# Performance work log

Measured on AMD Instinct MI355X. Metric: run time of the kernel, lower is better.

Reference implementation:

```python
import jax, jax.numpy as jnp
import numpy as np

N, D, K = 100000, 512, 32
H1, H2 = 512, 256
LN2PI_2 = float(np.log(2.0 * np.pi) / 2.0)


def _glorot(key, shape):
    fan_in, fan_out = shape[0], shape[1]
    limit = np.sqrt(6.0 / (fan_in + fan_out))
    return jax.random.uniform(key, shape, jnp.float32, -limit, limit)


def setup_inputs() -> dict:
    key = jax.random.key(0)
    k0, k1, k2, k3 = jax.random.split(key, 4)
    return {
        "x": jax.random.normal(k0, (N, D), jnp.float32),
        "W1": _glorot(k1, (D, H1)),
        "b1": jnp.zeros((H1,), jnp.float32),
        "W2": _glorot(k2, (H1, H2)),
        "b2": jnp.zeros((H2,), jnp.float32),
        "W3": _glorot(k3, (H2, K)),
        "b3": jnp.zeros((K,), jnp.float32),
    }


def reference(x, W1, b1, W2, b2, W3, b3):
    # instance attention MLP: softplus hiddens, softmax output -> [N, K]
    h = jax.nn.softplus(x @ W1 + b1)
    h = jax.nn.softplus(h @ W2 + b2)
    att = jax.nn.softmax(h @ W3 + b3, axis=-1)

    att_sum = jnp.sum(att, axis=0)  # [K]
    # weighted mean: sum_n x[n,d] * att[n,k] / sum_n att[n,k]  -> [K, D]
    means = (att.T @ x) / att_sum[:, None]
    # weighted variance: E_w[x^2] - mean^2 (algebraic expansion of
    # sum_n (x - mean)^2 * att / sum att, avoids [N,K,D] intermediate)
    ex2 = (att.T @ (x * x)) / att_sum[:, None]  # [K, D]
    vars_ = ex2 - means * means

    # GMM diagonal log-likelihood, expanded to GEMM form:
    inv_v = 1.0 / vars_  # [K, D]
    maha = (x * x) @ inv_v.T - 2.0 * (x @ (means * inv_v).T) \
           + jnp.sum(means * means * inv_v, axis=-1)[None, :]  # [N, K]
    gmm_log = -0.5 * maha - 0.5 * jnp.sum(jnp.log(vars_), axis=-1)[None, :] - D * LN2PI_2
    return gmm_log, vars_
```

## Files before the change

### kernel.cpp

```cpp
#include <hip/hip_runtime.h>
#include <hip/hip_bf16.h>
#include <math.h>

#define NROWS 100000
#define DDIM  512
#define KCL   32
#define H1DIM 512
#define H2DIM 256
#define LN2PI_2 0.9189385332046727f
#define NCHUNK 196
#define NPAD  100352
#define NBLK  784

typedef __attribute__((ext_vector_type(8))) short short8;
typedef __attribute__((ext_vector_type(4))) short shortx4;
typedef __attribute__((ext_vector_type(4))) float floatx4;

__device__ __forceinline__ float softplus_f(float v) {
    return fmaxf(v, 0.f) + __logf(1.f + __expf(-fabsf(v)));
}

__device__ __forceinline__ unsigned short f2bf_rne(float f) {
    unsigned int u = __float_as_uint(f);
    return (unsigned short)((u + 0x7fffu + ((u >> 16) & 1u)) >> 16);
}

__device__ __forceinline__ float bf2f(short v) {
    return __uint_as_float(((unsigned int)(unsigned short)v) << 16);
}

__global__ __launch_bounds__(256) void cvt_x_bf16(
    const float* __restrict__ x, short* __restrict__ xb)
{
    size_t i = ((size_t)blockIdx.x * 256 + threadIdx.x) * 8;
    float4 f0 = *(const float4*)&x[i];
    float4 f1 = *(const float4*)&x[i + 4];
    short8 o;
    o[0] = (short)f2bf_rne(f0.x); o[1] = (short)f2bf_rne(f0.y);
    o[2] = (short)f2bf_rne(f0.z); o[3] = (short)f2bf_rne(f0.w);
    o[4] = (short)f2bf_rne(f1.x); o[5] = (short)f2bf_rne(f1.y);
    o[6] = (short)f2bf_rne(f1.z); o[7] = (short)f2bf_rne(f1.w);
    *(short8*)&xb[i] = o;
}

__global__ __launch_bounds__(256) void cvt_weightT(
    const float* __restrict__ W, int Kd, int Nc, short* __restrict__ BT)
{
    int idx = blockIdx.x * 256 + threadIdx.x;
    if (idx >= Kd * Nc) return;
    int n = idx % Nc, k = idx / Nc;
    BT[(size_t)n * Kd + k] = (short)f2bf_rne(W[idx]);
}

#define LDP 40
__global__ __launch_bounds__(256) void gemm_bf16_softplus(
    const short* __restrict__ A, const short* __restrict__ BT,
    const float* __restrict__ bias, void* __restrict__ Cptr,
    int M, int Nc, int Kd, int out_bf16)
{
    __shared__ short As[2][128 * LDP];
    __shared__ short Bs[2][128 * LDP];

    const int tid = threadIdx.x;
    const int lid = tid & 63;
    const int w = tid >> 6;
    const int lm = lid & 15;
    const int lq = lid >> 4;
    const int wrow = (w & 1) * 64;
    const int wcol = (w >> 1) * 64;

    const int row0 = blockIdx.y * 128;
    const int col0 = blockIdx.x * 128;

    const int sr = tid >> 2;
    const int sc = (tid & 3) << 3;

    int gr0 = row0 + sr;       if (gr0 >= M) gr0 = M - 1;
    int gr1 = row0 + 64 + sr;  if (gr1 >= M) gr1 = M - 1;
    const short* Ar0 = A + (size_t)gr0 * Kd + sc;
    const short* Ar1 = A + (size_t)gr1 * Kd + sc;
    const short* Br0 = BT + (size_t)(col0 + sr) * Kd + sc;
    const short* Br1 = BT + (size_t)(col0 + 64 + sr) * Kd + sc;

    floatx4 acc[4][4];
    #pragma unroll
    for (int i = 0; i < 4; i++)
        #pragma unroll
        for (int j = 0; j < 4; j++)
            acc[i][j] = (floatx4){0.f, 0.f, 0.f, 0.f};

    short8 pa0, pa1, pb0, pb1;
    pa0 = *(const short8*)Ar0;
    pa1 = *(const short8*)Ar1;
    pb0 = *(const short8*)Br0;
    pb1 = *(const short8*)Br1;

    const int nk = Kd >> 5;
    for (int kt = 0; kt < nk; kt++) {
        const int buf = kt & 1;
        *(short8*)&As[buf][sr * LDP + sc]        = pa0;
        *(short8*)&As[buf][(64 + sr) * LDP + sc] = pa1;
        *(short8*)&Bs[buf][sr * LDP + sc]        = pb0;
        *(short8*)&Bs[buf][(64 + sr) * LDP + sc] = pb1;
        if (kt + 1 < nk) {
            int ko = (kt + 1) << 5;
            pa0 = *(const short8*)(Ar0 + ko);
            pa1 = *(const short8*)(Ar1 + ko);
            pb0 = *(const short8*)(Br0 + ko);
            pb1 = *(const short8*)(Br1 + ko);
        }
        __syncthreads();

        short8 a[4], b[4];
        #pragma unroll
        for (int i = 0; i < 4; i++)
            a[i] = *(const short8*)&As[buf][(wrow + i * 16 + lm) * LDP + lq * 8];
        #pragma unroll
        for (int j = 0; j < 4; j++)
            b[j] = *(const short8*)&Bs[buf][(wcol + j * 16 + lm) * LDP + lq * 8];
        #pragma unroll
        for (int i = 0; i < 4; i++)
            #pragma unroll
            for (int j = 0; j < 4; j++)
                acc[i][j] = __builtin_amdgcn_mfma_f32_16x16x32_bf16(
                    a[i], b[j], acc[i][j], 0, 0, 0);
    }

    float bb[4];
    #pragma unroll
    for (int j = 0; j < 4; j++)
        bb[j] = bias[col0 + wcol + j * 16 + lm];

    #pragma unroll
    for (int i = 0; i < 4; i++) {
        #pragma unroll
        for (int reg = 0; reg < 4; reg++) {
            int r = row0 + wrow + i * 16 + lq * 4 + reg;
            if (r < M) {
                #pragma unroll
                for (int j = 0; j < 4; j++) {
                    int c = col0 + wcol + j * 16 + lm;
                    float v = softplus_f(acc[i][j][reg] + bb[j]);
                    if (out_bf16)
                        ((short*)Cptr)[(size_t)r * Nc + c] = (short)f2bf_rne(v);
                    else
                        ((float*)Cptr)[(size_t)r * Nc + c] = v;
                }
            }
        }
    }
}

__global__ __launch_bounds__(256) void logits_mfma(
    const short* __restrict__ h2b, const short* __restrict__ W3T,
    const float* __restrict__ b3, short* __restrict__ attT,
    float* __restrict__ Patt)
{
    __shared__ short Ts[32][136];
    __shared__ float red[4][32];

    const int tid = threadIdx.x;
    const int lane = tid & 63;
    const int lm = lane & 15;
    const int lq = lane >> 4;
    const int w = tid >> 6;
    const int wrow = w * 32;
    const int row0 = blockIdx.x * 128;

    short8 bf[2][8];
    #pragma unroll
    for (int j = 0; j < 2; j++)
        #pragma unroll
        for (int s = 0; s < 8; s++)
            bf[j][s] = *(const short8*)&W3T[(j * 16 + lm) * H2DIM + s * 32 + lq * 8];

    int gr0 = row0 + wrow + lm;      if (gr0 >= NROWS) gr0 = NROWS - 1;
    int gr1 = row0 + wrow + 16 + lm; if (gr1 >= NROWS) gr1 = NROWS - 1;
    const short* a0p = h2b + (size_t)gr0 * H2DIM + lq * 8;
    const short* a1p = h2b + (size_t)gr1 * H2DIM + lq * 8;

    floatx4 acc[2][2];
    #pragma unroll
    for (int i = 0; i < 2; i++)
        #pragma unroll
        for (int j = 0; j < 2; j++)
            acc[i][j] = (floatx4){0.f, 0.f, 0.f, 0.f};

    #pragma unroll
    for (int s = 0; s < 8; s++) {
        short8 a0 = *(const short8*)(a0p + s * 32);
        short8 a1 = *(const short8*)(a1p + s * 32);
        acc[0][0] = __builtin_amdgcn_mfma_f32_16x16x32_bf16(a0, bf[0][s], acc[0][0], 0, 0, 0);
        acc[0][1] = __builtin_amdgcn_mfma_f32_16x16x32_bf16(a0, bf[1][s], acc[0][1], 0, 0, 0);
        acc[1][0] = __builtin_amdgcn_mfma_f32_16x16x32_bf16(a1, bf[0][s], acc[1][0], 0, 0, 0);
        acc[1][1] = __builtin_amdgcn_mfma_f32_16x16x32_bf16(a1, bf[1][s], acc[1][1], 0, 0, 0);
    }

    const float b3v0 = b3[lm];
    const float b3v1 = b3[16 + lm];

    float p0 = 0.f, p1 = 0.f;

    #pragma unroll
    for (int i = 0; i < 2; i++) {
        #pragma unroll
        for (int reg = 0; reg < 4; reg++) {
            const int rloc = wrow + i * 16 + lq * 4 + reg;
            const int rg = row0 + rloc;
            float v0 = acc[i][0][reg] + b3v0;
            float v1 = acc[i][1][reg] + b3v1;
            float m = fmaxf(v0, v1);
            m = fmaxf(m, __shfl_xor(m, 1));
            m = fmaxf(m, __shfl_xor(m, 2));
            m = fmaxf(m, __shfl_xor(m, 4));
            m = fmaxf(m, __shfl_xor(m, 8));
            float e0 = __expf(v0 - m);
            float e1 = __expf(v1 - m);
            float sm = e0 + e1;
            sm += __shfl_xor(sm, 1);
            sm += __shfl_xor(sm, 2);
            sm += __shfl_xor(sm, 4);
            sm += __shfl_xor(sm, 8);
            float inv = 1.f / sm;
            e0 *= inv; e1 *= inv;
            if (rg >= NROWS) { e0 = 0.f; e1 = 0.f; }
            p0 += e0; p1 += e1;
            Ts[lm][rloc]      = (short)f2bf_rne(e0);
            Ts[16 + lm][rloc] = (short)f2bf_rne(e1);
        }
    }

    p0 += __shfl_xor(p0, 16); p0 += __shfl_xor(p0, 32);
    p1 += __shfl_xor(p1, 16); p1 += __shfl_xor(p1, 32);
    if (lq == 0) { red[w][lm] = p0; red[w][16 + lm] = p1; }

    __syncthreads();

    if (tid < KCL)
        Patt[blockIdx.x * KCL + tid] =
            red[0][tid] + red[1][tid] + red[2][tid] + red[3][tid];

    #pragma unroll
    for (int p = 0; p < 2; p++) {
        int u = p * 256 + tid;
        int r = u >> 4;
        int cs = (u & 15) << 3;
        short8 o = *(const short8*)&Ts[r][cs];
        *(short8*)&attT[(size_t)r * NPAD + row0 + cs] = o;
    }
}

__global__ __launch_bounds__(256, 4) void stats_mfma(
    const float* __restrict__ x, const short* __restrict__ attT,
    float* __restrict__ P)
{
    __shared__ short xT[32 * 512];

    const int tid = threadIdx.x;
    const int lane = tid & 63;
    const int lm = lane & 15;
    const int lq = lane >> 4;
    const int w = tid >> 6;
    const int kh = w >> 1;
    const int dh = w & 1;

    const int cblk = blockIdx.x;
    const int dgrp = blockIdx.y;
    const int n0 = cblk * 512;

    short8 afrag[16];
    const short* arow = attT + (size_t)(kh * 16 + lm) * NPAD + n0 + lq * 8;
    #pragma unroll
    for (int s = 0; s < 16; s++)
        afrag[s] = *(const short8*)(arow + s * 32);

    const int c = tid & 31;
    const int rq = tid >> 5;
    const bool full = (n0 + 512 <= NROWS);

    for (int dt = 0; dt < 4; dt++) {
        const int colf = dgrp * 128 + dt * 32 + c;
        __syncthreads();
        if (full) {
            const float* xp = x + (size_t)n0 * DDIM + colf;
            #pragma unroll 4
            for (int p = 0; p < 16; p++) {
                int r = p * 32 + rq * 4;
                float f0 = xp[(size_t)(r + 0) * DDIM];
                float f1 = xp[(size_t)(r + 1) * DDIM];
                float f2 = xp[(size_t)(r + 2) * DDIM];
                float f3 = xp[(size_t)(r + 3) * DDIM];
                unsigned int u01 = (unsigned int)f2bf_rne(f0) |
                                   ((unsigned int)f2bf_rne(f1) << 16);
                unsigned int u23 = (unsigned int)f2bf_rne(f2) |
                                   ((unsigned int)f2bf_rne(f3) << 16);
                int boff = (c << 10) + ((r * 2) ^ ((c & 15) << 4));
                *(uint2*)((char*)xT + boff) = make_uint2(u01, u23);
            }
        } else {
            #pragma unroll 4
            for (int p = 0; p < 16; p++) {
                int r = p * 32 + rq * 4;
                int g0 = min(n0 + r + 0, NROWS - 1);
                int g1 = min(n0 + r + 1, NROWS - 1);
                int g2 = min(n0 + r + 2, NROWS - 1);
                int g3 = min(n0 + r + 3, NROWS - 1);
                float f0 = x[(size_t)g0 * DDIM + colf];
                float f1 = x[(size_t)g1 * DDIM + colf];
                float f2 = x[(size_t)g2 * DDIM + colf];
                float f3 = x[(size_t)g3 * DDIM + colf];
                unsigned int u01 = (unsigned int)f2bf_rne(f0) |
                                   ((unsigned int)f2bf_rne(f1) << 16);
                unsigned int u23 = (unsigned int)f2bf_rne(f2) |
                                   ((unsigned int)f2bf_rne(f3) << 16);
                int boff = (c << 10) + ((r * 2) ^ ((c & 15) << 4));
                *(uint2*)((char*)xT + boff) = make_uint2(u01, u23);
            }
        }
        __syncthreads();

        floatx4 acc1 = (floatx4){0.f, 0.f, 0.f, 0.f};
        floatx4 acc2 = (floatx4){0.f, 0.f, 0.f, 0.f};
        const int rowb = (dh * 16 + lm) << 10;
        #pragma unroll
        for (int s = 0; s < 16; s++) {
            int boff = rowb + ((s * 64 + lq * 16) ^ (lm << 4));
            short8 bx = *(const short8*)((const char*)xT + boff);
            union { short8 s8; unsigned int u[4]; } bq;
            #pragma unroll
            for (int e = 0; e < 4; e++) {
                float f0 = bf2f(bx[2 * e]);
                float f1 = bf2f(bx[2 * e + 1]);
                f0 *= f0; f1 *= f1;
                bq.u[e] = (unsigned int)f2bf_rne(f0) |
                          ((unsigned int)f2bf_rne(f1) << 16);
            }
            acc1 = __builtin_amdgcn_mfma_f32_16x16x32_bf16(
                afrag[s], bx, acc1, 0, 0, 0);
            acc2 = __builtin_amdgcn_mfma_f32_16x16x32_bf16(
                afrag[s], bq.s8, acc2, 0, 0, 0);
        }

        const size_t pbase = (size_t)cblk * 32768 +
                             (size_t)(kh * 16 + lq * 4) * 512 +
                             (size_t)(dgrp * 128 + dt * 32 + dh * 16 + lm);
        #pragma unroll
        for (int reg = 0; reg < 4; reg++) {
            P[pbase + (size_t)reg * 512]         = acc1[reg];
            P[pbase + 16384 + (size_t)reg * 512] = acc2[reg];
        }
    }
}

__global__ __launch_bounds__(256) void stats_reduce(
    const float* __restrict__ P, const float* __restrict__ Patt,
    float* __restrict__ S12, float* __restrict__ att_sum)
{
    int e = blockIdx.x * 256 + threadIdx.x;
    float sum = 0.f;
    for (int cc = 0; cc < NCHUNK; cc++)
        sum += P[(size_t)cc * 32768 + e];
    S12[e] = sum;

    if (blockIdx.x == 0 && threadIdx.x < KCL) {
        float as = 0.f;
        for (int cc = 0; cc < NBLK; cc++) as += Patt[cc * KCL + threadIdx.x];
        att_sum[threadIdx.x] = as;
    }
}

__global__ __launch_bounds__(256) void finalize_stats(
    const float* __restrict__ S12, const float* __restrict__ att_sum,
    short* __restrict__ Bp, float* __restrict__ konst,
    float* __restrict__ vars_out)
{
    int k = blockIdx.x;
    int tid = threadIdx.x;
    __shared__ float red[256];

    float inv_as = 1.f / att_sum[k];
    float csum = 0.f, lsum = 0.f;
    for (int d = tid; d < DDIM; d += 256) {
        float mean = S12[k * DDIM + d] * inv_as;
        float ex2  = S12[KCL * DDIM + k * DDIM + d] * inv_as;
        float var  = ex2 - mean * mean;
        vars_out[k * DDIM + d] = var;
        float iv = 1.f / var;
        Bp[(size_t)k * 1024 + d]       = (short)f2bf_rne(-0.5f * iv);
        Bp[(size_t)k * 1024 + 512 + d] = (short)f2bf_rne(mean * iv);
        csum += mean * mean * iv;
        lsum += logf(var);
    }
    red[tid] = csum;
    __syncthreads();
    for (int s = 128; s > 0; s >>= 1) {
        if (tid < s) red[tid] += red[tid + s];
        __syncthreads();
    }
    float ctot = red[0];
    __syncthreads();
    red[tid] = lsum;
    __syncthreads();
    for (int s = 128; s > 0; s >>= 1) {
        if (tid < s) red[tid] += red[tid + s];
        __syncthreads();
    }
    if (tid == 0)
        konst[k] = -0.5f * ctot - 0.5f * red[0] - DDIM * LN2PI_2;
}

#define LDG 40
__global__ __launch_bounds__(256) void gmm_out_mfma(
    const float* __restrict__ x, const short* __restrict__ Bp,
    const float* __restrict__ konst, float* __restrict__ out)
{
    __shared__ short As_sq[256 * LDG];
    __shared__ short As_x[256 * LDG];

    const int tid = threadIdx.x;
    const int lane = tid & 63;
    const int lm = lane & 15;
    const int lq = lane >> 4;
    const int wid = tid >> 6;
    const int row0 = blockIdx.x * 256;

    floatx4 acc[4][2];
    #pragma unroll
    for (int i = 0; i < 4; i++)
        #pragma unroll
        for (int j = 0; j < 2; j++)
            acc[i][j] = (floatx4){0.f, 0.f, 0.f, 0.f};

    for (int dt = 0; dt < 16; dt++) {
        __syncthreads();
        #pragma unroll
        for (int h = 0; h < 8; h++) {
            int u = tid + h * 256;
            int r = u >> 3;
            int seg = (u & 7) << 2;
            int gr = row0 + r;
            float4 v = make_float4(0.f, 0.f, 0.f, 0.f);
            if (gr < NROWS)
                v = *(const float4*)&x[(size_t)gr * DDIM + dt * 32 + seg];
            shortx4 sx, sq;
            sx[0] = (short)f2bf_rne(v.x); sq[0] = (short)f2bf_rne(v.x * v.x);
            sx[1] = (short)f2bf_rne(v.y); sq[1] = (short)f2bf_rne(v.y * v.y);
            sx[2] = (short)f2bf_rne(v.z); sq[2] = (short)f2bf_rne(v.z * v.z);
            sx[3] = (short)f2bf_rne(v.w); sq[3] = (short)f2bf_rne(v.w * v.w);
            *(shortx4*)&As_x[r * LDG + seg]  = sx;
            *(shortx4*)&As_sq[r * LDG + seg] = sq;
        }
        __syncthreads();

        short8 a_sq[4], a_x[4], b_sq[2], b_x[2];
        #pragma unroll
        for (int i = 0; i < 4; i++) {
            int off = (wid * 64 + i * 16 + lm) * LDG + lq * 8;
            a_sq[i] = *(const short8*)&As_sq[off];
            a_x[i]  = *(const short8*)&As_x[off];
        }
        #pragma unroll
        for (int j = 0; j < 2; j++) {
            const size_t bo = (size_t)(j * 16 + lm) * 1024 + dt * 32 + lq * 8;
            b_sq[j] = *(const short8*)&Bp[bo];
            b_x[j]  = *(const short8*)&Bp[bo + 512];
        }
        #pragma unroll
        for (int i = 0; i < 4; i++)
            #pragma unroll
            for (int j = 0; j < 2; j++) {
                acc[i][j] = __builtin_amdgcn_mfma_f32_16x16x32_bf16(
                    a_sq[i], b_sq[j], acc[i][j], 0, 0, 0);
                acc[i][j] = __builtin_amdgcn_mfma_f32_16x16x32_bf16(
                    a_x[i], b_x[j], acc[i][j], 0, 0, 0);
            }
    }

    float kst[2];
    kst[0] = konst[lm];
    kst[1] = konst[16 + lm];

    #pragma unroll
    for (int i = 0; i < 4; i++) {
        #pragma unroll
        for (int reg = 0; reg < 4; reg++) {
            int r = row0 + wid * 64 + i * 16 + lq * 4 + reg;
            if (r < NROWS) {
                out[(size_t)r * KCL + lm]      = acc[i][0][reg] + kst[0];
                out[(size_t)r * KCL + 16 + lm] = acc[i][1][reg] + kst[1];
            }
        }
    }
}

extern "C" void kernel_launch(void* const* d_in, const int* in_sizes, int n_in,
                              void* d_out, int out_size, void* d_ws, size_t ws_size,
                              hipStream_t stream)
{
    const float* x  = (const float*)d_in[0];
    const float* W1 = (const float*)d_in[1];
    const float* b1 = (const float*)d_in[2];
    const float* W2 = (const float*)d_in[3];
    const float* b2 = (const float*)d_in[4];
    const float* W3 = (const float*)d_in[5];
    const float* b3 = (const float*)d_in[6];
    float* out = (float*)d_out;

    short* h1b     = (short*)d_ws;
    float* h2      = (float*)(h1b + (size_t)NROWS * H1DIM);
    float* att     = h2 + (size_t)NROWS * H2DIM;
    float* P       = att + (size_t)NROWS * KCL;
    float* PattOld = P + (size_t)NCHUNK * 32768;
    float* S12     = PattOld + NCHUNK * KCL;
    float* att_sum = S12 + 2 * KCL * DDIM;
    short* Bp      = (short*)(att_sum + KCL);
    float* konst   = (float*)(Bp + KCL * 1024);
    (void)ws_size; (void)in_sizes; (void)n_in; (void)out_size; (void)PattOld;

    short* xb   = (short*)h2;
    short* h2b  = (short*)h2;
    short* W1T = (short*)P;
    short* W2T = W1T + H1DIM * DDIM;
    short* W3T = W2T + H2DIM * H1DIM;
    short* attT = h1b;
    float* PattN = att;

    cvt_x_bf16<<<dim3(NROWS * DDIM / 2048), 256, 0, stream>>>(x, xb);
    cvt_weightT<<<dim3((DDIM * H1DIM + 255) / 256), 256, 0, stream>>>(
        W1, DDIM, H1DIM, W1T);
    cvt_weightT<<<dim3((H1DIM * H2DIM + 255) / 256), 256, 0, stream>>>(
        W2, H1DIM, H2DIM, W2T);
    cvt_weightT<<<dim3((H2DIM * KCL + 255) / 256), 256, 0, stream>>>(
        W3, H2DIM, KCL, W3T);

    int mblocks = (NROWS + 127) / 128;

    gemm_bf16_softplus<<<dim3(H1DIM / 128, mblocks), 256, 0, stream>>>(
        xb, W1T, b1, (void*)h1b, NROWS, H1DIM, DDIM, 1);
    gemm_bf16_softplus<<<dim3(H2DIM / 128, mblocks), 256, 0, stream>>>(
        h1b, W2T, b2, (void*)h2b, NROWS, H2DIM, H1DIM, 1);
    logits_mfma<<<dim3(NBLK), 256, 0, stream>>>(h2b, W3T, b3, attT, PattN);
    stats_mfma<<<dim3(NCHUNK, 4), 256, 0, stream>>>(x, attT, P);
    stats_reduce<<<dim3(128), 256, 0, stream>>>(P, PattN, S12, att_sum);
    finalize_stats<<<dim3(KCL), 256, 0, stream>>>(
        S12, att_sum, Bp, konst, out + (size_t)NROWS * KCL);
    gmm_out_mfma<<<dim3((NROWS + 255) / 256), 256, 0, stream>>>(x, Bp, konst, out);
}
```

Baseline: 688.2 us.

## Fuse x bf16 conversion into first GEMM, merge weight casts, XCD-aware block remap

```diff
diff --git a/kernel.cpp b/kernel.cpp
--- a/kernel.cpp
+++ b/kernel.cpp
@@ -29,32 +29,42 @@
     return __uint_as_float(((unsigned int)(unsigned short)v) << 16);
 }
 
-__global__ __launch_bounds__(256) void cvt_x_bf16(
-    const float* __restrict__ x, short* __restrict__ xb)
-{
-    size_t i = ((size_t)blockIdx.x * 256 + threadIdx.x) * 8;
-    float4 f0 = *(const float4*)&x[i];
-    float4 f1 = *(const float4*)&x[i + 4];
-    short8 o;
-    o[0] = (short)f2bf_rne(f0.x); o[1] = (short)f2bf_rne(f0.y);
-    o[2] = (short)f2bf_rne(f0.z); o[3] = (short)f2bf_rne(f0.w);
-    o[4] = (short)f2bf_rne(f1.x); o[5] = (short)f2bf_rne(f1.y);
-    o[6] = (short)f2bf_rne(f1.z); o[7] = (short)f2bf_rne(f1.w);
-    *(short8*)&xb[i] = o;
-}
-
-__global__ __launch_bounds__(256) void cvt_weightT(
-    const float* __restrict__ W, int Kd, int Nc, short* __restrict__ BT)
+__device__ __forceinline__ short8 cvt8(float4 a, float4 b) {
+    union { unsigned int u[4]; short8 s; } r;
+    asm("v_cvt_pk_bf16_f32 %0, %1, %2" : "=v"(r.u[0]) : "v"(a.x), "v"(a.y));
+    asm("v_cvt_pk_bf16_f32 %0, %1, %2" : "=v"(r.u[1]) : "v"(a.z), "v"(a.w));
+    asm("v_cvt_pk_bf16_f32 %0, %1, %2" : "=v"(r.u[2]) : "v"(b.x), "v"(b.y));
+    asm("v_cvt_pk_bf16_f32 %0, %1, %2" : "=v"(r.u[3]) : "v"(b.z), "v"(b.w));
+    return r.s;
+}
+
+__global__ __launch_bounds__(256) void cvt_weights(
+    const float* __restrict__ W1, const float* __restrict__ W2,
+    const float* __restrict__ W3, short* __restrict__ W1T,
+    short* __restrict__ W2T, short* __restrict__ W3T)
 {
     int idx = blockIdx.x * 256 + threadIdx.x;
-    if (idx >= Kd * Nc) return;
-    int n = idx % Nc, k = idx / Nc;
-    BT[(size_t)n * Kd + k] = (short)f2bf_rne(W[idx]);
+    const int n1 = DDIM * H1DIM;
+    const int n2 = H1DIM * H2DIM;
+    const int n3 = H2DIM * KCL;
+    if (idx < n1) {
+        int n = idx % H1DIM, k = idx / H1DIM;
+        W1T[(size_t)n * DDIM + k] = (short)f2bf_rne(W1[idx]);
+    } else if (idx < n1 + n2) {
+        int rel = idx - n1;
+        int n = rel % H2DIM, k = rel / H2DIM;
+        W2T[(size_t)n * H1DIM + k] = (short)f2bf_rne(W2[rel]);
+    } else if (idx < n1 + n2 + n3) {
+        int rel = idx - n1 - n2;
+        int n = rel % KCL, k = rel / KCL;
+        W3T[(size_t)n * H2DIM + k] = (short)f2bf_rne(W3[rel]);
+    }
 }
 
 #define LDP 40
-__global__ __launch_bounds__(256) void gemm_bf16_softplus(
-    const short* __restrict__ A, const short* __restrict__ BT,
+template<int AFP32>
+__global__ __launch_bounds__(256) void gemm_sp(
+    const void* __restrict__ Aptr, const short* __restrict__ BT,
     const float* __restrict__ bias, void* __restrict__ Cptr,
     int M, int Nc, int Kd, int out_bf16)
 {
@@ -69,16 +79,24 @@
     const int wrow = (w & 1) * 64;
     const int wcol = (w >> 1) * 64;
 
-    const int row0 = blockIdx.y * 128;
-    const int col0 = blockIdx.x * 128;
+    const int nwg = gridDim.x * gridDim.y;
+    const int bid = blockIdx.y * gridDim.x + blockIdx.x;
+    const int q = nwg >> 3, r = nwg & 7;
+    const int xcd = bid & 7, slot = bid >> 3;
+    const int L = (xcd < r ? xcd * (q + 1) : r * (q + 1) + (xcd - r) * q) + slot;
+    const int row0 = (L / gridDim.x) * 128;
+    const int col0 = (L % gridDim.x) * 128;
 
     const int sr = tid >> 2;
     const int sc = (tid & 3) << 3;
 
     int gr0 = row0 + sr;       if (gr0 >= M) gr0 = M - 1;
     int gr1 = row0 + 64 + sr;  if (gr1 >= M) gr1 = M - 1;
-    const short* Ar0 = A + (size_t)gr0 * Kd + sc;
-    const short* Ar1 = A + (size_t)gr1 * Kd + sc;
+
+    const float* Ar0f = (const float*)Aptr + (size_t)gr0 * Kd + sc;
+    const float* Ar1f = (const float*)Aptr + (size_t)gr1 * Kd + sc;
+    const short* Ar0s = (const short*)Aptr + (size_t)gr0 * Kd + sc;
+    const short* Ar1s = (const short*)Aptr + (size_t)gr1 * Kd + sc;
     const short* Br0 = BT + (size_t)(col0 + sr) * Kd + sc;
     const short* Br1 = BT + (size_t)(col0 + 64 + sr) * Kd + sc;
 
@@ -89,23 +107,41 @@
         for (int j = 0; j < 4; j++)
             acc[i][j] = (floatx4){0.f, 0.f, 0.f, 0.f};
 
+    float4 fa0, fa1, fa2, fa3;
     short8 pa0, pa1, pb0, pb1;
-    pa0 = *(const short8*)Ar0;
-    pa1 = *(const short8*)Ar1;
+    if constexpr (AFP32) {
+        fa0 = *(const float4*)Ar0f; fa1 = *(const float4*)(Ar0f + 4);
+        fa2 = *(const float4*)Ar1f; fa3 = *(const float4*)(Ar1f + 4);
+    } else {
+        pa0 = *(const short8*)Ar0s;
+        pa1 = *(const short8*)Ar1s;
+    }
     pb0 = *(const short8*)Br0;
     pb1 = *(const short8*)Br1;
 
     const int nk = Kd >> 5;
     for (int kt = 0; kt < nk; kt++) {
         const int buf = kt & 1;
-        *(short8*)&As[buf][sr * LDP + sc]        = pa0;
-        *(short8*)&As[buf][(64 + sr) * LDP + sc] = pa1;
+        if constexpr (AFP32) {
+            *(short8*)&As[buf][sr * LDP + sc]        = cvt8(fa0, fa1);
+            *(short8*)&As[buf][(64 + sr) * LDP + sc] = cvt8(fa2, fa3);
+        } else {
+            *(short8*)&As[buf][sr * LDP + sc]        = pa0;
+            *(short8*)&As[buf][(64 + sr) * LDP + sc] = pa1;
+        }
         *(short8*)&Bs[buf][sr * LDP + sc]        = pb0;
         *(short8*)&Bs[buf][(64 + sr) * LDP + sc] = pb1;
         if (kt + 1 < nk) {
             int ko = (kt + 1) << 5;
-            pa0 = *(const short8*)(Ar0 + ko);
-            pa1 = *(const short8*)(Ar1 + ko);
+            if constexpr (AFP32) {
+                fa0 = *(const float4*)(Ar0f + ko);
+                fa1 = *(const float4*)(Ar0f + ko + 4);
+                fa2 = *(const float4*)(Ar1f + ko);
+                fa3 = *(const float4*)(Ar1f + ko + 4);
+            } else {
+                pa0 = *(const short8*)(Ar0s + ko);
+                pa1 = *(const short8*)(Ar1s + ko);
+            }
             pb0 = *(const short8*)(Br0 + ko);
             pb1 = *(const short8*)(Br1 + ko);
         }
@@ -135,16 +171,16 @@
     for (int i = 0; i < 4; i++) {
         #pragma unroll
         for (int reg = 0; reg < 4; reg++) {
-            int r = row0 + wrow + i * 16 + lq * 4 + reg;
-            if (r < M) {
+            int rr = row0 + wrow + i * 16 + lq * 4 + reg;
+            if (rr < M) {
                 #pragma unroll
                 for (int j = 0; j < 4; j++) {
                     int c = col0 + wcol + j * 16 + lm;
                     float v = softplus_f(acc[i][j][reg] + bb[j]);
                     if (out_bf16)
-                        ((short*)Cptr)[(size_t)r * Nc + c] = (short)f2bf_rne(v);
+                        ((short*)Cptr)[(size_t)rr * Nc + c] = (short)f2bf_rne(v);
                     else
-                        ((float*)Cptr)[(size_t)r * Nc + c] = v;
+                        ((float*)Cptr)[(size_t)rr * Nc + c] = v;
                 }
             }
         }
@@ -243,10 +279,10 @@
     #pragma unroll
     for (int p = 0; p < 2; p++) {
         int u = p * 256 + tid;
-        int r = u >> 4;
+        int rr = u >> 4;
         int cs = (u & 15) << 3;
-        short8 o = *(const short8*)&Ts[r][cs];
-        *(short8*)&attT[(size_t)r * NPAD + row0 + cs] = o;
+        short8 o = *(const short8*)&Ts[rr][cs];
+        *(short8*)&attT[(size_t)rr * NPAD + row0 + cs] = o;
     }
 }
 
@@ -285,26 +321,26 @@
             const float* xp = x + (size_t)n0 * DDIM + colf;
             #pragma unroll 4
             for (int p = 0; p < 16; p++) {
-                int r = p * 32 + rq * 4;
-                float f0 = xp[(size_t)(r + 0) * DDIM];
-                float f1 = xp[(size_t)(r + 1) * DDIM];
-                float f2 = xp[(size_t)(r + 2) * DDIM];
-                float f3 = xp[(size_t)(r + 3) * DDIM];
+                int rr = p * 32 + rq * 4;
+                float f0 = xp[(size_t)(rr + 0) * DDIM];
+                float f1 = xp[(size_t)(rr + 1) * DDIM];
+                float f2 = xp[(size_t)(rr + 2) * DDIM];
+                float f3 = xp[(size_t)(rr + 3) * DDIM];
                 unsigned int u01 = (unsigned int)f2bf_rne(f0) |
                                    ((unsigned int)f2bf_rne(f1) << 16);
                 unsigned int u23 = (unsigned int)f2bf_rne(f2) |
                                    ((unsigned int)f2bf_rne(f3) << 16);
-                int boff = (c << 10) + ((r * 2) ^ ((c & 15) << 4));
+                int boff = (c << 10) + ((rr * 2) ^ ((c & 15) << 4));
                 *(uint2*)((char*)xT + boff) = make_uint2(u01, u23);
             }
         } else {
             #pragma unroll 4
             for (int p = 0; p < 16; p++) {
-                int r = p * 32 + rq * 4;
-                int g0 = min(n0 + r + 0, NROWS - 1);
-                int g1 = min(n0 + r + 1, NROWS - 1);
-                int g2 = min(n0 + r + 2, NROWS - 1);
-                int g3 = min(n0 + r + 3, NROWS - 1);
+                int rr = p * 32 + rq * 4;
+                int g0 = min(n0 + rr + 0, NROWS - 1);
+                int g1 = min(n0 + rr + 1, NROWS - 1);
+                int g2 = min(n0 + rr + 2, NROWS - 1);
+                int g3 = min(n0 + rr + 3, NROWS - 1);
                 float f0 = x[(size_t)g0 * DDIM + colf];
                 float f1 = x[(size_t)g1 * DDIM + colf];
                 float f2 = x[(size_t)g2 * DDIM + colf];
@@ -313,7 +349,7 @@
                                    ((unsigned int)f2bf_rne(f1) << 16);
                 unsigned int u23 = (unsigned int)f2bf_rne(f2) |
                                    ((unsigned int)f2bf_rne(f3) << 16);
-                int boff = (c << 10) + ((r * 2) ^ ((c & 15) << 4));
+                int boff = (c << 10) + ((rr * 2) ^ ((c & 15) << 4));
                 *(uint2*)((char*)xT + boff) = make_uint2(u01, u23);
             }
         }
@@ -436,9 +472,9 @@
         #pragma unroll
         for (int h = 0; h < 8; h++) {
             int u = tid + h * 256;
-            int r = u >> 3;
+            int rr = u >> 3;
             int seg = (u & 7) << 2;
-            int gr = row0 + r;
+            int gr = row0 + rr;
             float4 v = make_float4(0.f, 0.f, 0.f, 0.f);
             if (gr < NROWS)
                 v = *(const float4*)&x[(size_t)gr * DDIM + dt * 32 + seg];
@@ -447,8 +483,8 @@
             sx[1] = (short)f2bf_rne(v.y); sq[1] = (short)f2bf_rne(v.y * v.y);
             sx[2] = (short)f2bf_rne(v.z); sq[2] = (short)f2bf_rne(v.z * v.z);
             sx[3] = (short)f2bf_rne(v.w); sq[3] = (short)f2bf_rne(v.w * v.w);
-            *(shortx4*)&As_x[r * LDG + seg]  = sx;
-            *(shortx4*)&As_sq[r * LDG + seg] = sq;
+            *(shortx4*)&As_x[rr * LDG + seg]  = sx;
+            *(shortx4*)&As_sq[rr * LDG + seg] = sq;
         }
         __syncthreads();
 
@@ -484,10 +520,10 @@
     for (int i = 0; i < 4; i++) {
         #pragma unroll
         for (int reg = 0; reg < 4; reg++) {
-            int r = row0 + wid * 64 + i * 16 + lq * 4 + reg;
-            if (r < NROWS) {
-                out[(size_t)r * KCL + lm]      = acc[i][0][reg] + kst[0];
-                out[(size_t)r * KCL + 16 + lm] = acc[i][1][reg] + kst[1];
+            int rr = row0 + wid * 64 + i * 16 + lq * 4 + reg;
+            if (rr < NROWS) {
+                out[(size_t)rr * KCL + lm]      = acc[i][0][reg] + kst[0];
+                out[(size_t)rr * KCL + 16 + lm] = acc[i][1][reg] + kst[1];
             }
         }
     }
@@ -517,7 +553,6 @@
     float* konst   = (float*)(Bp + KCL * 1024);
     (void)ws_size; (void)in_sizes; (void)n_in; (void)out_size; (void)PattOld;
 
-    short* xb   = (short*)h2;
     short* h2b  = (short*)h2;
     short* W1T = (short*)P;
     short* W2T = W1T + H1DIM * DDIM;
@@ -525,20 +560,14 @@
     short* attT = h1b;
     float* PattN = att;
 
-    cvt_x_bf16<<<dim3(NROWS * DDIM / 2048), 256, 0, stream>>>(x, xb);
-    cvt_weightT<<<dim3((DDIM * H1DIM + 255) / 256), 256, 0, stream>>>(
-        W1, DDIM, H1DIM, W1T);
-    cvt_weightT<<<dim3((H1DIM * H2DIM + 255) / 256), 256, 0, stream>>>(
-        W2, H1DIM, H2DIM, W2T);
-    cvt_weightT<<<dim3((H2DIM * KCL + 255) / 256), 256, 0, stream>>>(
-        W3, H2DIM, KCL, W3T);
+    cvt_weights<<<dim3(1568), 256, 0, stream>>>(W1, W2, W3, W1T, W2T, W3T);
 
     int mblocks = (NROWS + 127) / 128;
 
-    gemm_bf16_softplus<<<dim3(H1DIM / 128, mblocks), 256, 0, stream>>>(
-        xb, W1T, b1, (void*)h1b, NROWS, H1DIM, DDIM, 1);
-    gemm_bf16_softplus<<<dim3(H2DIM / 128, mblocks), 256, 0, stream>>>(
-        h1b, W2T, b2, (void*)h2b, NROWS, H2DIM, H1DIM, 1);
+    gemm_sp<1><<<dim3(H1DIM / 128, mblocks), 256, 0, stream>>>(
+        (const void*)x, W1T, b1, (void*)h1b, NROWS, H1DIM, DDIM, 1);
+    gemm_sp<0><<<dim3(H2DIM / 128, mblocks), 256, 0, stream>>>(
+        (const void*)h1b, W2T, b2, (void*)h2b, NROWS, H2DIM, H1DIM, 1);
     logits_mfma<<<dim3(NBLK), 256, 0, stream>>>(h2b, W3T, b3, attT, PattN);
     stats_mfma<<<dim3(NCHUNK, 4), 256, 0, stream>>>(x, attT, P);
     stats_reduce<<<dim3(128), 256, 0, stream>>>(P, PattN, S12, att_sum);
```

New measurement: 658.4 us. 4.3% less time.
